# Kernel tuning notes

Measured on AMD Instinct MI355X. Metric: run time of the kernel, lower is better.

Reference implementation:

```python
import jax, jax.numpy as jnp
import numpy as np

B, A, G, C, P, PH, PW = 8, 19248, 32, 81, 32, 138, 138
K_POS = 128            # fixed upper bound on positives used for the mask loss
INPUT_SIZE = 550.0
POS_THR, NEG_THR = 0.5, 0.4
ALPHA, GAMMA = 0.25, 2.0
NEG_POS_RATIO = 3
CLS_W, BOX_W, MASK_W = 1.0, 1.5, 6.125
VAR_XY, VAR_WH = 0.1, 0.2
EPS = 1e-6


def setup_inputs() -> dict:
    key = jax.random.key(0)
    ks = jax.random.split(key, 10)
    class_preds = jax.random.normal(ks[0], (B, A, C), jnp.float32)
    box_preds = jax.random.normal(ks[1], (B, A, 4), jnp.float32) * 0.1
    mask_coeffs = jax.random.normal(ks[2], (B, A, P), jnp.float32)
    prototypes = jax.random.normal(ks[3], (B, P, PH, PW), jnp.float32)
    # anchors in normalized [cx, cy, w, h]
    cxy = jax.random.uniform(ks[4], (A, 2), jnp.float32)
    wh = jax.random.uniform(ks[5], (A, 2), jnp.float32) * 0.25 + 0.02
    anchors = jnp.concatenate([cxy, wh], axis=-1)
    # GT boxes in absolute pixels [x1, y1, x2, y2] within 550x550
    xy1 = jax.random.uniform(ks[6], (B, G, 2), jnp.float32) * 380.0
    bwh = jax.random.uniform(ks[7], (B, G, 2), jnp.float32) * 150.0 + 15.0
    gt_boxes = jnp.concatenate([xy1, xy1 + bwh], axis=-1)
    gt_labels = jax.random.randint(ks[8], (B, G), 1, C)  # foreground classes
    gt_masks = (jax.random.uniform(ks[9], (B, G, PH, PW)) > 0.5).astype(jnp.float32)
    return {
        "class_preds": class_preds, "box_preds": box_preds,
        "mask_coeffs": mask_coeffs, "prototypes": prototypes,
        "anchors": anchors, "gt_boxes": gt_boxes,
        "gt_labels": gt_labels, "gt_masks": gt_masks,
    }


def _iou(a, b):
    # a: (A,4) xyxy, b: (G,4) xyxy -> (A,G)
    max_xy = jnp.minimum(a[:, None, 2:], b[None, :, 2:])
    min_xy = jnp.maximum(a[:, None, :2], b[None, :, :2])
    inter = jnp.clip(max_xy - min_xy, 0.0).prod(-1)
    area_a = (a[:, 2] - a[:, 0]) * (a[:, 3] - a[:, 1])
    area_b = (b[:, 2] - b[:, 0]) * (b[:, 3] - b[:, 1])
    union = area_a[:, None] + area_b[None, :] - inter
    return inter / jnp.clip(union, EPS)


def _smooth_l1(x):
    d = jnp.abs(x)
    return jnp.where(d < 1.0, 0.5 * d * d, d - 0.5)


def _image_loss(cls_p, box_p, coeffs, protos, gtb, gtl, gtm, anchors, anchors_xyxy):
    gtb = gtb / INPUT_SIZE                           # normalize to [0,1]
    iou = _iou(anchors_xyxy, gtb)                    # (A, G)
    best_gt_iou = iou.max(axis=1)                    # (A,)
    best_gt_idx = iou.argmax(axis=1)                 # (A,)
    best_anchor_idx = iou.argmax(axis=0)             # (G,) bipartite guarantee

    pos = best_gt_iou >= POS_THR
    pos = pos.at[best_anchor_idx].set(True)
    best_gt_idx = best_gt_idx.at[best_anchor_idx].set(jnp.arange(G))
    neg = (best_gt_iou < NEG_THR) & ~pos
    num_pos = pos.sum()
    # deterministic hard-negative cap at neg:pos = 3:1 (orig. uses randperm)
    neg = neg & (jnp.cumsum(neg) <= num_pos * NEG_POS_RATIO)

    matched_labels = jnp.where(pos, gtl[best_gt_idx], 0)   # 0 = background
    mb = gtb[best_gt_idx]                                  # (A,4) matched xyxy
    posf = pos.astype(jnp.float32)

    # ---- focal classification loss over pos|neg anchors ----
    probs = jax.nn.softmax(cls_p, axis=-1)
    p_t = jnp.take_along_axis(probs, matched_labels[:, None], axis=1)[:, 0]
    p_t = jnp.clip(p_t, EPS, 1.0 - EPS)
    alpha_t = jnp.where(matched_labels > 0, ALPHA, 1.0 - ALPHA)
    focal = alpha_t * (1.0 - p_t) ** GAMMA * (-jnp.log(p_t))
    cls_loss = (focal * (pos | neg).astype(jnp.float32)).sum()

    acx, acy, aw, ah = anchors[:, 0], anchors[:, 1], anchors[:, 2], anchors[:, 3]
    gcx = 0.5 * (mb[:, 0] + mb[:, 2]); gcy = 0.5 * (mb[:, 1] + mb[:, 3])
    gw = jnp.clip(mb[:, 2] - mb[:, 0], EPS); gh = jnp.clip(mb[:, 3] - mb[:, 1], EPS)
    t = jnp.stack([
        (gcx - acx) / (aw * VAR_XY),
        (gcy - acy) / (ah * VAR_XY),
        jnp.log(gw / aw) / VAR_WH,
        jnp.log(gh / ah) / VAR_WH,
    ], axis=-1)                                            # (A,4)
    box_loss = (_smooth_l1(box_p - t).sum(-1) * posf).sum()

    # ---- BCE mask loss on (up to K_POS) positive anchors ----
    score = jnp.where(pos, best_gt_iou + 1.0, 0.0)
    _, idx = jax.lax.top_k(score, K_POS)                   # (K,)
    w = posf[idx]                                          # 0-weight padding
    logits = jnp.einsum('kp,phw->khw', coeffs[idx], protos)  # (K,PH,PW)
    tgt = gtm[best_gt_idx[idx]]                            # (K,PH,PW)
    bce = jnp.maximum(logits, 0.0) - logits * tgt + jnp.log1p(jnp.exp(-jnp.abs(logits)))
    mask_loss = (bce.mean(axis=(1, 2)) * w).sum()

    return cls_loss, box_loss, mask_loss, num_pos


def reference(class_preds, box_preds, mask_coeffs, prototypes, anchors, gt_boxes, gt_labels, gt_masks):
    a_xyxy = jnp.concatenate(
        [anchors[:, :2] - anchors[:, 2:] * 0.5, anchors[:, :2] + anchors[:, 2:] * 0.5], axis=-1)
    cls_l, box_l, mask_l, npos = jax.vmap(
        _image_loss, in_axes=(0, 0, 0, 0, 0, 0, 0, None, None)
    )(class_preds, box_preds, mask_coeffs, prototypes, gt_boxes, gt_labels, gt_masks, anchors, a_xyxy)
    denom = jnp.maximum(npos.sum(), 1).astype(jnp.float32)
    total = (CLS_W * cls_l.sum() + BOX_W * box_l.sum() + MASK_W * mask_l.sum()) / denom
    return total
```

## Files before the change

### kernel.cpp

```cpp
#include <hip/hip_runtime.h>
#include <math.h>

#define BB 8
#define AA 19248
#define GG 32
#define CC 81
#define PP 32
#define PHW 19044
#define KPOS 128
#define NEGRATIO 3
#define SELCAP 7680
#define NWCH 304
#define NB1 76
#define NB0 75
#define NPT 1191
#define NB7 298
#define NB45 24

typedef _Float16 half8 __attribute__((ext_vector_type(8)));
typedef float floatx4 __attribute__((ext_vector_type(4)));

__device__ __forceinline__ float iou_one(float ax1, float ay1, float ax2, float ay2,
                                         float areaA,
                                         float gx1, float gy1, float gx2, float gy2) {
#pragma clang fp contract(off)
    float ix1 = fmaxf(ax1, gx1), iy1 = fmaxf(ay1, gy1);
    float ix2 = fminf(ax2, gx2), iy2 = fminf(ay2, gy2);
    float iw = fmaxf(ix2 - ix1, 0.0f), ih = fmaxf(iy2 - iy1, 0.0f);
    float inter = iw * ih;
    float areaB = (gx2 - gx1) * (gy2 - gy1);
    float u = areaA + areaB - inter;
    u = fmaxf(u, 1e-6f);
    return inter / u;
}

__global__ __launch_bounds__(256) void k01(
    const float* __restrict__ anchors, const float* __restrict__ gt_boxes,
    const float* __restrict__ protos, const float* __restrict__ gtm,
    float* __restrict__ best_iou, int* __restrict__ best_g,
    unsigned long long* __restrict__ gkey_part, float* __restrict__ acc,
    _Float16* __restrict__ protoT, unsigned* __restrict__ pmask) {
#pragma clang fp contract(off)
    int b = blockIdx.y;
    __shared__ float sg[GG][4];
    __shared__ unsigned long long s_gk[GG];

    if (blockIdx.x >= NB1) {
        int px = (blockIdx.x - NB1) * 256 + threadIdx.x;
        if (px >= PHW) return;
        const float* pb = protos + (size_t)b * PP * PHW + px;
        _Float16 v[PP];
        #pragma unroll
        for (int k = 0; k < PP; ++k)
            v[k] = (_Float16)pb[(size_t)k * PHW];
        half8* dst = (half8*)&protoT[((size_t)b * PHW + px) * PP];
        #pragma unroll
        for (int q = 0; q < 4; ++q)
            dst[q] = *(half8*)&v[q * 8];
        const float* gb = gtm + (size_t)b * GG * PHW + px;
        unsigned m = 0u;
        #pragma unroll
        for (int g = 0; g < GG; ++g)
            m |= (gb[(size_t)g * PHW] > 0.5f) ? (1u << g) : 0u;
        pmask[(size_t)b * PHW + px] = m;
        return;
    }

    int a = blockIdx.x * 256 + threadIdx.x;
    int lane = threadIdx.x & 63;
    if (blockIdx.x == 0 && b == 0 && threadIdx.x < 4)
        ((int*)acc)[threadIdx.x] = 0;
    for (int t = threadIdx.x; t < GG * 4; t += 256)
        sg[t >> 2][t & 3] = gt_boxes[b * GG * 4 + t] / 550.0f;
    if (threadIdx.x < GG) s_gk[threadIdx.x] = 0ULL;
    __syncthreads();
    bool valid = a < AA;
    int ac = valid ? a : AA - 1;
    float4 an = ((const float4*)anchors)[ac];
    float ax1 = an.x - an.z * 0.5f, ay1 = an.y - an.w * 0.5f;
    float ax2 = an.x + an.z * 0.5f, ay2 = an.y + an.w * 0.5f;
    float areaA = (ax2 - ax1) * (ay2 - ay1);
    unsigned long long bk = 0ULL;
    for (int gg = 0; gg < GG; ++gg) {
        int g = (gg + lane) & (GG - 1);
        float v = iou_one(ax1, ay1, ax2, ay2, areaA, sg[g][0], sg[g][1], sg[g][2], sg[g][3]);
        unsigned vb = __float_as_uint(v);
        unsigned long long k2 = ((unsigned long long)vb << 6) | (unsigned)(GG - 1 - g);
        if (k2 > bk) bk = k2;
        if (valid) {
            unsigned long long kg =
                ((unsigned long long)vb << 32) | (unsigned)(AA - 1 - a);
            atomicMax(&s_gk[g], kg);
        }
    }
    if (valid) {
        best_iou[b * AA + a] = __uint_as_float((unsigned)(bk >> 6));
        best_g[b * AA + a] = (GG - 1) - (int)(bk & 63ULL);
    }
    __syncthreads();
    if (threadIdx.x < GG)
        gkey_part[((size_t)b * NB1 + blockIdx.x) * GG + threadIdx.x] = s_gk[threadIdx.x];
}

__global__ __launch_bounds__(1024) void k36(
    const float* __restrict__ best_iou, const int* __restrict__ best_g_in,
    const unsigned long long* __restrict__ gkey_part, const int* __restrict__ gtl,
    int* __restrict__ gidx_out, int* __restrict__ selmask,
    unsigned long long* __restrict__ pos_key,
    int* __restrict__ pos_cnt, int* __restrict__ g_npos,
    int* __restrict__ act_list, int* __restrict__ act_cnt,
    const float* __restrict__ coeffs,
    int* __restrict__ sel_g, _Float16* __restrict__ sel_coef,
    int* __restrict__ sel_cnt) {
#pragma clang fp contract(off)
    int b = blockIdx.x;
    int tid = threadIdx.x;
    int lane = tid & 63, wid = tid >> 6;
    __shared__ short s_ov[AA];
    __shared__ unsigned long long s_gmax[GG];
    __shared__ int sba[GG];
    __shared__ int s_gtl[GG];
    __shared__ unsigned long long s_pmask[NWCH];
    __shared__ unsigned long long s_nmask[NWCH];
    __shared__ int s_woff[NWCH];
    __shared__ int s_wred[5];
    __shared__ int s_cnt, s_act;
    __shared__ unsigned long long s_keys[SELCAP];
    __shared__ int s_hist[256];
    __shared__ int s_sfx[256];
    __shared__ int s_wsum[4];
    __shared__ unsigned long long s_prefix;
    __shared__ int s_kk;
    __shared__ int s_nsel;
    __shared__ int s_sel_a[KPOS];
    __shared__ int s_sorted_a[KPOS];
    __shared__ int s_sorted_g[KPOS];
    __shared__ int s_gcnt[GG];

    for (int i = tid; i < AA; i += 1024) s_ov[i] = -1;
    if (tid < GG) { s_gmax[tid] = 0ULL; s_gtl[tid] = gtl[b * GG + tid]; }
    if (tid == 0) { s_cnt = 0; s_act = 0; s_prefix = 0ULL; s_kk = KPOS; s_nsel = 0; }
    __syncthreads();
    for (int c = tid >> 5; c < NB1; c += 32)
        atomicMax(&s_gmax[tid & 31],
                  gkey_part[((size_t)b * NB1 + c) * GG + (tid & 31)]);
    __syncthreads();
    if (tid < GG) sba[tid] = AA - 1 - (int)(unsigned)(s_gmax[tid] & 0xffffffffULL);
    __syncthreads();
    if (tid == 0) {
        for (int g = 0; g < GG; ++g) s_ov[sba[g]] = (short)g;
    }
    __syncthreads();

    for (int base = 0; base < AA; base += 1024) {
        int a = base + tid;
        bool p = false, npre = false;
        if (a < AA) {
            float biou = best_iou[b * AA + a];
            int ov = s_ov[a];
            int gi = (ov >= 0) ? ov : best_g_in[b * AA + a];
            p = (biou >= 0.5f) || (ov >= 0);
            npre = (biou < 0.4f) && !p;
            gidx_out[b * AA + a] = gi;
            selmask[b * AA + a] = p ? 2 : (npre ? 1 : 0);
            if (p) {
                int slot = atomicAdd(&s_cnt, 1);
                unsigned vb = __float_as_uint(biou + 1.0f);
                unsigned long long key =
                    ((unsigned long long)(vb - 0x3F800000u) << 32) |
                    (unsigned)(AA - 1 - a);
                pos_key[(size_t)b * AA + slot] = key;
                if (slot < SELCAP) s_keys[slot] = key;
            }
        }
        unsigned long long pm = __ballot(p);
        unsigned long long nm = __ballot(npre);
        if (lane == 0) {
            int w = (base >> 6) + wid;
            s_pmask[w] = pm;
            s_nmask[w] = nm;
        }
    }
    __syncthreads();
    int npos = s_cnt;
    if (tid == 0) { pos_cnt[b] = npos; atomicAdd(g_npos, npos); }
    int cap = npos * NEGRATIO;

    int c = (tid < NWCH) ? __popcll(s_nmask[tid]) : 0;
    int inc = c;
    if (wid < 5) {
        #pragma unroll
        for (int d = 1; d < 64; d <<= 1) {
            int t = __shfl_up(inc, d);
            if (lane >= d) inc += t;
        }
        if (lane == 63) s_wred[wid] = inc;
    }
    __syncthreads();
    if (tid == 0) {
        int run = 0;
        #pragma unroll
        for (int i = 0; i < 5; ++i) { int t = s_wred[i]; s_wred[i] = run; run += t; }
    }
    __syncthreads();
    if (tid < NWCH) s_woff[tid] = inc - c + s_wred[wid];
    __syncthreads();

    for (int base = 0; base < AA; base += 1024) {
        int a = base + tid;
        int w = (base >> 6) + wid;
        unsigned long long nm = s_nmask[w], pm = s_pmask[w];
        bool npre = (nm >> lane) & 1ULL;
        bool pos  = (pm >> lane) & 1ULL;
        int rank = __popcll(nm & ((1ULL << lane) - 1ULL));
        bool kept = npre && (s_woff[w] + rank + 1 <= cap);
        if (a < AA) {
            if (npre && !kept) selmask[b * AA + a] = 0;
            if (pos || kept) {
                int slot = atomicAdd(&s_act, 1);
                int gi = gidx_out[b * AA + a];
                int lbl = pos ? s_gtl[gi] : 0;
                unsigned e = (unsigned)a | ((unsigned)gi << 15) |
                             ((unsigned)lbl << 20) | (pos ? 0x80000000u : 0u);
                act_list[b * AA + slot] = (int)e;
            }
        }
    }
    __syncthreads();
    if (tid == 0) act_cnt[b] = s_act;

    int n = npos;
    int K = (n < KPOS) ? n : KPOS;
    const unsigned long long* keys =
        (n <= SELCAP) ? s_keys : (pos_key + (size_t)b * AA);
    __syncthreads();

    if (n > KPOS) {
        for (int d = 6; d >= 0; --d) {
            unsigned long long pref = s_prefix;
            int kk = s_kk;
            if (tid < 256) s_hist[tid] = 0;
            __syncthreads();
            unsigned long long mhi = ~((1ULL << (8 * (d + 1))) - 1ULL);
            for (int i = tid; i < n; i += 1024) {
                unsigned long long k = keys[i];
                if ((k & mhi) == pref)
                    atomicAdd(&s_hist[(int)((k >> (8 * d)) & 255)], 1);
            }
            __syncthreads();
            int x = 0;
            if (tid < 256) {
                x = s_hist[255 - tid];
                #pragma unroll
                for (int o = 1; o < 64; o <<= 1) {
                    int t = __shfl_up(x, o);
                    if (lane >= o) x += t;
                }
                if (lane == 63) s_wsum[tid >> 6] = x;
            }
            __syncthreads();
            if (tid == 0) {
                int run = 0;
                #pragma unroll
                for (int i = 0; i < 4; ++i) { int t = s_wsum[i]; s_wsum[i] = run; run += t; }
            }
            __syncthreads();
            if (tid < 256) s_sfx[255 - tid] = x + s_wsum[tid >> 6];
            __syncthreads();
            if (tid < 256) {
                int v = tid;
                int ge = s_sfx[v];
                int gt = (v == 255) ? 0 : s_sfx[v + 1];
                if (ge >= kk && gt < kk) {
                    s_prefix = pref | ((unsigned long long)v << (8 * d));
                    s_kk = kk - gt;
                }
            }
            __syncthreads();
        }
    }

    unsigned long long T = (n > KPOS) ? s_prefix : 0ULL;
    for (int i = tid; i < n; i += 1024) {
        unsigned long long k = keys[i];
        if (k >= T) {
            int slot = atomicAdd(&s_nsel, 1);
            if (slot < KPOS)
                s_sel_a[slot] = AA - 1 - (int)(unsigned)(k & 0xffffffffu);
        }
    }
    __syncthreads();

    if (tid < GG) s_gcnt[tid] = 0;
    __syncthreads();
    int mya = -1, myg = -1;
    if (tid < K) {
        mya = s_sel_a[tid];
        myg = gidx_out[b * AA + mya];
        atomicAdd(&s_gcnt[myg], 1);
    }
    __syncthreads();
    if (tid == 0) {
        int run = 0;
        for (int g = 0; g < GG; ++g) { int cg = s_gcnt[g]; s_gcnt[g] = run; run += cg; }
    }
    __syncthreads();
    if (tid < K) {
        int pos = atomicAdd(&s_gcnt[myg], 1);
        s_sorted_a[pos] = mya;
        s_sorted_g[pos] = myg;
    }
    __syncthreads();

    if (tid == 0) sel_cnt[b] = K;
    int glast = (K > 0) ? s_sorted_g[K - 1] : 0;
    for (int t = tid; t < KPOS * PP; t += 1024) {
        int k = t >> 5, p = t & 31;
        _Float16 v = (_Float16)0.0f;
        if (k < K) {
            int a = s_sorted_a[k];
            v = (_Float16)coeffs[((size_t)(b * AA + a)) * PP + p];
        }
        sel_coef[(size_t)(b * KPOS + k) * PP + p] = v;
    }
    for (int t = tid; t < KPOS; t += 1024)
        sel_g[b * KPOS + t] = (t < K) ? s_sorted_g[t] : glast;
}

__global__ __launch_bounds__(256) void k457(
    const float* __restrict__ cls_p, const int* __restrict__ act_list,
    const int* __restrict__ act_cnt, const float* __restrict__ box_p,
    const float* __restrict__ anchors, const float* __restrict__ gt_boxes,
    float* __restrict__ part_cls, float* __restrict__ part_box,
    const _Float16* __restrict__ protoT, const unsigned* __restrict__ pmask,
    const _Float16* __restrict__ sel_coef, const int* __restrict__ sel_g,
    const int* __restrict__ sel_cnt, float* __restrict__ part_mask) {
    int b = blockIdx.y;
    int tid = threadIdx.x;

    if (blockIdx.x < NB45) {
        int n = act_cnt[b];
        float fsum = 0.0f, bsum = 0.0f;
        for (int i = blockIdx.x * 256 + tid; i < n; i += NB45 * 256) {
            unsigned e = (unsigned)act_list[b * AA + i];
            int a = e & 0x7fff;
            int g = (e >> 15) & 31;
            int lbl = (e >> 20) & 127;
            bool pos = (e >> 31) != 0u;
            const float* x = cls_p + (size_t)(b * AA + a) * CC;
            float v80 = x[80];
            float m0 = v80, m1 = -3.0e38f, m2 = -3.0e38f, m3 = -3.0e38f;
            #pragma unroll
            for (int q = 0; q < 20; ++q) {
                m0 = fmaxf(m0, x[4 * q + 0]); m1 = fmaxf(m1, x[4 * q + 1]);
                m2 = fmaxf(m2, x[4 * q + 2]); m3 = fmaxf(m3, x[4 * q + 3]);
            }
            float m = fmaxf(fmaxf(m0, m1), fmaxf(m2, m3));
            float s0 = __expf(v80 - m), s1 = 0.f, s2 = 0.f, s3 = 0.f;
            #pragma unroll
            for (int q = 0; q < 20; ++q) {
                s0 += __expf(x[4 * q + 0] - m); s1 += __expf(x[4 * q + 1] - m);
                s2 += __expf(x[4 * q + 2] - m); s3 += __expf(x[4 * q + 3] - m);
            }
            float s = (s0 + s1) + (s2 + s3);
            float pt = __expf(x[lbl] - m) / s;
            pt = fminf(fmaxf(pt, 1e-6f), 1.0f - 1e-6f);
            float at = (lbl > 0) ? 0.25f : 0.75f;
            float om = 1.0f - pt;
            fsum += at * om * om * (-__logf(pt));
            if (pos) {
#pragma clang fp contract(off)
                float4 mb = ((const float4*)gt_boxes)[b * GG + g];
                float4 an = ((const float4*)anchors)[a];
                const float4 bp = ((const float4*)box_p)[(size_t)b * AA + a];
                float q0 = mb.x / 550.0f, q1 = mb.y / 550.0f;
                float q2 = mb.z / 550.0f, q3 = mb.w / 550.0f;
                float gcx = 0.5f * (q0 + q2), gcy = 0.5f * (q1 + q3);
                float gw = fmaxf(q2 - q0, 1e-6f), gh = fmaxf(q3 - q1, 1e-6f);
                float t0 = (gcx - an.x) / (an.z * 0.1f);
                float t1 = (gcy - an.y) / (an.w * 0.1f);
                float t2 = logf(gw / an.z) / 0.2f;
                float t3 = logf(gh / an.w) / 0.2f;
                float d;
                d = fabsf(bp.x - t0); bsum += (d < 1.0f) ? 0.5f * d * d : d - 0.5f;
                d = fabsf(bp.y - t1); bsum += (d < 1.0f) ? 0.5f * d * d : d - 0.5f;
                d = fabsf(bp.z - t2); bsum += (d < 1.0f) ? 0.5f * d * d : d - 0.5f;
                d = fabsf(bp.w - t3); bsum += (d < 1.0f) ? 0.5f * d * d : d - 0.5f;
            }
        }
        for (int off = 32; off; off >>= 1) {
            fsum += __shfl_xor(fsum, off);
            bsum += __shfl_xor(bsum, off);
        }
        __shared__ float s4f[4], s4b[4];
        if ((tid & 63) == 0) { s4f[tid >> 6] = fsum; s4b[tid >> 6] = bsum; }
        __syncthreads();
        if (tid == 0) {
            part_cls[b * NB45 + blockIdx.x] = s4f[0] + s4f[1] + s4f[2] + s4f[3];
            part_box[b * NB45 + blockIdx.x] = s4b[0] + s4b[1] + s4b[2] + s4b[3];
        }
        return;
    }

    int nk = sel_cnt[b];
    int wave = tid >> 6, lane = tid & 63;
    int lg = lane >> 4;
    int ln = lane & 15;
    int pt = (blockIdx.x - NB45) * 4 + wave;
    int px = pt * 16 + ln;
    bool pxv = (pt < NPT) && (px < PHW);
    int pc = pxv ? px : PHW - 1;

    half8 bfrag = *(const half8*)&protoT[((size_t)b * PHW + pc) * PP + lg * 8];
    unsigned gmask = pmask[(size_t)b * PHW + pc];

    const _Float16* ca = sel_coef + (size_t)b * KPOS * PP;
    const int* gb = sel_g + b * KPOS;

    half8 af[8];
    int4 gv[8];
    #pragma unroll
    for (int kt = 0; kt < 8; ++kt) {
        af[kt] = *(const half8*)&ca[(size_t)(kt * 16 + ln) * PP + lg * 8];
        gv[kt] = *(const int4*)&gb[kt * 16 + lg * 4];
    }

    float acc = 0.0f;
    #pragma unroll
    for (int kt = 0; kt < 8; ++kt) {
        floatx4 c = {0.f, 0.f, 0.f, 0.f};
        c = __builtin_amdgcn_mfma_f32_16x16x32_f16(af[kt], bfrag, c, 0, 0, 0);
        #pragma unroll
        for (int r = 0; r < 4; ++r) {
            int k = kt * 16 + lg * 4 + r;
            float l = c[r];
            int g0 = (r == 0) ? gv[kt].x : (r == 1) ? gv[kt].y
                   : (r == 2) ? gv[kt].z : gv[kt].w;
            float t = (float)((gmask >> g0) & 1u);
            float bce = fmaxf(l, 0.f) - l * t + __logf(1.f + __expf(-fabsf(l)));
            if (pxv && k < nk) acc += bce;
        }
    }

    for (int off = 32; off; off >>= 1) acc += __shfl_xor(acc, off);
    __shared__ float s_red[4];
    if (lane == 0) s_red[wave] = acc;
    __syncthreads();
    if (tid == 0)
        part_mask[(size_t)b * NB7 + (blockIdx.x - NB45)] =
            s_red[0] + s_red[1] + s_red[2] + s_red[3];
}

__global__ __launch_bounds__(1024) void k8_final(
    const float* __restrict__ part_cls, const float* __restrict__ part_box,
    const float* __restrict__ part_mask, const int* __restrict__ npos,
    float* __restrict__ out) {
    int tid = threadIdx.x;
    float c = 0.f, bx = 0.f, mk = 0.f;
    for (int i = tid; i < NB45 * BB; i += 1024) {
        c += part_cls[i];
        bx += part_box[i];
    }
    for (int i = tid; i < NB7 * BB; i += 1024)
        mk += part_mask[i];
    for (int off = 32; off; off >>= 1) {
        c += __shfl_xor(c, off);
        bx += __shfl_xor(bx, off);
        mk += __shfl_xor(mk, off);
    }
    __shared__ float sc[16], sb[16], sm[16];
    if ((tid & 63) == 0) {
        sc[tid >> 6] = c; sb[tid >> 6] = bx; sm[tid >> 6] = mk;
    }
    __syncthreads();
    if (tid == 0) {
        float tc = 0.f, tb = 0.f, tm = 0.f;
        #pragma unroll
        for (int i = 0; i < 16; ++i) { tc += sc[i]; tb += sb[i]; tm += sm[i]; }
        float denom = fmaxf((float)(*npos), 1.0f);
        out[0] = (1.0f * tc + 1.5f * tb + 6.125f * (tm / (float)PHW)) / denom;
    }
}

extern "C" void kernel_launch(void* const* d_in, const int* in_sizes, int n_in,
                              void* d_out, int out_size, void* d_ws, size_t ws_size,
                              hipStream_t stream) {
    (void)in_sizes; (void)n_in; (void)out_size; (void)ws_size;
    const float* class_preds = (const float*)d_in[0];
    const float* box_preds   = (const float*)d_in[1];
    const float* mask_coeffs = (const float*)d_in[2];
    const float* prototypes  = (const float*)d_in[3];
    const float* anchors     = (const float*)d_in[4];
    const float* gt_boxes    = (const float*)d_in[5];
    const int*   gt_labels   = (const int*)d_in[6];
    const float* gt_masks    = (const float*)d_in[7];
    float* out = (float*)d_out;

    size_t off = 0;
    char* w = (char*)d_ws;
    auto take = [&](size_t bytes) -> char* {
        char* p = w + off;
        off += (bytes + 255) & ~(size_t)255;
        return p;
    };
    float* acc      = (float*)take(32);
    float* best_iou = (float*)take((size_t)BB * AA * 4);
    int*   best_g   = (int*)  take((size_t)BB * AA * 4);
    int*   gidx     = (int*)  take((size_t)BB * AA * 4);
    int*   selmask  = (int*)  take((size_t)BB * AA * 4);
    unsigned long long* gkey_part =
        (unsigned long long*)take((size_t)BB * NB1 * GG * 8);
    int*   pos_cnt  = (int*)  take((size_t)BB * 4);
    unsigned long long* pos_key = (unsigned long long*)take((size_t)BB * AA * 8);
    int*   sel_g    = (int*)  take((size_t)BB * KPOS * 4);
    int*   sel_cnt  = (int*)  take((size_t)BB * 4);
    _Float16* sel_coef = (_Float16*)take((size_t)BB * KPOS * PP * 2);
    int*   act_list = (int*)  take((size_t)BB * AA * 4);
    int*   act_cnt  = (int*)  take((size_t)BB * 4);
    _Float16* protoT = (_Float16*)take((size_t)BB * PHW * PP * 2);
    unsigned* pmaskb = (unsigned*)take((size_t)BB * PHW * 4);
    float* part_cls  = (float*)take((size_t)BB * NB45 * 4);
    float* part_box  = (float*)take((size_t)BB * NB45 * 4);
    float* part_mask = (float*)take((size_t)BB * NB7 * 4);

    k01<<<dim3(NB1 + NB0, BB), 256, 0, stream>>>(
        anchors, gt_boxes, prototypes, gt_masks,
        best_iou, best_g, gkey_part, acc, protoT, pmaskb);
    k36<<<BB, 1024, 0, stream>>>(
        best_iou, best_g, gkey_part, gt_labels, gidx, selmask, pos_key, pos_cnt,
        (int*)(acc + 3), act_list, act_cnt,
        mask_coeffs, sel_g, sel_coef, sel_cnt);
    k457<<<dim3(NB45 + NB7, BB), 256, 0, stream>>>(
        class_preds, act_list, act_cnt, box_preds, anchors, gt_boxes,
        part_cls, part_box,
        protoT, pmaskb, sel_coef, sel_g, sel_cnt, part_mask);
    k8_final<<<1, 1024, 0, stream>>>(
        part_cls, part_box, part_mask, (int*)(acc + 3), out);
}
```

Before: 71.96 us.

## Pack best IoU/gt into one key, keep gt index in LDS, fold final reduction

k01 now writes a single 64-bit packed key per anchor instead of separate best_iou and best_g arrays. k36 keeps the matched gt index in shared memory and drops the global gidx and selmask arrays and the shared key cache. The final reduction kernel is removed; the last k457 block, detected through an atomic done counter, does the final sum. This cuts global traffic and one kernel launch, but top-k selection now always reads keys from global memory.

```diff
diff --git a/kernel.cpp b/kernel.cpp
--- a/kernel.cpp
+++ b/kernel.cpp
@@ -9,13 +9,13 @@
 #define PHW 19044
 #define KPOS 128
 #define NEGRATIO 3
-#define SELCAP 7680
 #define NWCH 304
 #define NB1 76
 #define NB0 75
 #define NPT 1191
 #define NB7 298
 #define NB45 24
+#define NTOT ((NB45 + NB7) * BB)
 
 typedef _Float16 half8 __attribute__((ext_vector_type(8)));
 typedef float floatx4 __attribute__((ext_vector_type(4)));
@@ -37,7 +37,7 @@
 __global__ __launch_bounds__(256) void k01(
     const float* __restrict__ anchors, const float* __restrict__ gt_boxes,
     const float* __restrict__ protos, const float* __restrict__ gtm,
-    float* __restrict__ best_iou, int* __restrict__ best_g,
+    unsigned long long* __restrict__ best_key,
     unsigned long long* __restrict__ gkey_part, float* __restrict__ acc,
     _Float16* __restrict__ protoT, unsigned* __restrict__ pmask) {
 #pragma clang fp contract(off)
@@ -93,30 +93,27 @@
             atomicMax(&s_gk[g], kg);
         }
     }
-    if (valid) {
-        best_iou[b * AA + a] = __uint_as_float((unsigned)(bk >> 6));
-        best_g[b * AA + a] = (GG - 1) - (int)(bk & 63ULL);
-    }
+    if (valid) best_key[(size_t)b * AA + a] = bk;
     __syncthreads();
     if (threadIdx.x < GG)
         gkey_part[((size_t)b * NB1 + blockIdx.x) * GG + threadIdx.x] = s_gk[threadIdx.x];
 }
 
 __global__ __launch_bounds__(1024) void k36(
-    const float* __restrict__ best_iou, const int* __restrict__ best_g_in,
+    const unsigned long long* __restrict__ best_key,
     const unsigned long long* __restrict__ gkey_part, const int* __restrict__ gtl,
-    int* __restrict__ gidx_out, int* __restrict__ selmask,
     unsigned long long* __restrict__ pos_key,
     int* __restrict__ pos_cnt, int* __restrict__ g_npos,
     int* __restrict__ act_list, int* __restrict__ act_cnt,
     const float* __restrict__ coeffs,
     int* __restrict__ sel_g, _Float16* __restrict__ sel_coef,
-    int* __restrict__ sel_cnt) {
+    int* __restrict__ sel_cnt, int* __restrict__ done_ctr) {
 #pragma clang fp contract(off)
     int b = blockIdx.x;
     int tid = threadIdx.x;
     int lane = tid & 63, wid = tid >> 6;
     __shared__ short s_ov[AA];
+    __shared__ short s_gi[AA];
     __shared__ unsigned long long s_gmax[GG];
     __shared__ int sba[GG];
     __shared__ int s_gtl[GG];
@@ -125,7 +122,6 @@
     __shared__ int s_woff[NWCH];
     __shared__ int s_wred[5];
     __shared__ int s_cnt, s_act;
-    __shared__ unsigned long long s_keys[SELCAP];
     __shared__ int s_hist[256];
     __shared__ int s_sfx[256];
     __shared__ int s_wsum[4];
@@ -139,7 +135,10 @@
 
     for (int i = tid; i < AA; i += 1024) s_ov[i] = -1;
     if (tid < GG) { s_gmax[tid] = 0ULL; s_gtl[tid] = gtl[b * GG + tid]; }
-    if (tid == 0) { s_cnt = 0; s_act = 0; s_prefix = 0ULL; s_kk = KPOS; s_nsel = 0; }
+    if (tid == 0) {
+        s_cnt = 0; s_act = 0; s_prefix = 0ULL; s_kk = KPOS; s_nsel = 0;
+        if (b == 0) *done_ctr = 0;
+    }
     __syncthreads();
     for (int c = tid >> 5; c < NB1; c += 32)
         atomicMax(&s_gmax[tid & 31],
@@ -156,13 +155,14 @@
         int a = base + tid;
         bool p = false, npre = false;
         if (a < AA) {
-            float biou = best_iou[b * AA + a];
+            unsigned long long bk = best_key[(size_t)b * AA + a];
+            float biou = __uint_as_float((unsigned)(bk >> 6));
+            int bg = (GG - 1) - (int)(bk & 63ULL);
             int ov = s_ov[a];
-            int gi = (ov >= 0) ? ov : best_g_in[b * AA + a];
+            int gi = (ov >= 0) ? ov : bg;
             p = (biou >= 0.5f) || (ov >= 0);
             npre = (biou < 0.4f) && !p;
-            gidx_out[b * AA + a] = gi;
-            selmask[b * AA + a] = p ? 2 : (npre ? 1 : 0);
+            s_gi[a] = (short)gi;
             if (p) {
                 int slot = atomicAdd(&s_cnt, 1);
                 unsigned vb = __float_as_uint(biou + 1.0f);
@@ -170,7 +170,6 @@
                     ((unsigned long long)(vb - 0x3F800000u) << 32) |
                     (unsigned)(AA - 1 - a);
                 pos_key[(size_t)b * AA + slot] = key;
-                if (slot < SELCAP) s_keys[slot] = key;
             }
         }
         unsigned long long pm = __ballot(p);
@@ -214,16 +213,13 @@
         bool pos  = (pm >> lane) & 1ULL;
         int rank = __popcll(nm & ((1ULL << lane) - 1ULL));
         bool kept = npre && (s_woff[w] + rank + 1 <= cap);
-        if (a < AA) {
-            if (npre && !kept) selmask[b * AA + a] = 0;
-            if (pos || kept) {
-                int slot = atomicAdd(&s_act, 1);
-                int gi = gidx_out[b * AA + a];
-                int lbl = pos ? s_gtl[gi] : 0;
-                unsigned e = (unsigned)a | ((unsigned)gi << 15) |
-                             ((unsigned)lbl << 20) | (pos ? 0x80000000u : 0u);
-                act_list[b * AA + slot] = (int)e;
-            }
+        if (a < AA && (pos || kept)) {
+            int slot = atomicAdd(&s_act, 1);
+            int gi = s_gi[a];
+            int lbl = pos ? s_gtl[gi] : 0;
+            unsigned e = (unsigned)a | ((unsigned)gi << 15) |
+                         ((unsigned)lbl << 20) | (pos ? 0x80000000u : 0u);
+            act_list[b * AA + slot] = (int)e;
         }
     }
     __syncthreads();
@@ -231,8 +227,7 @@
 
     int n = npos;
     int K = (n < KPOS) ? n : KPOS;
-    const unsigned long long* keys =
-        (n <= SELCAP) ? s_keys : (pos_key + (size_t)b * AA);
+    const unsigned long long* keys = pos_key + (size_t)b * AA;
     __syncthreads();
 
     if (n > KPOS) {
@@ -296,7 +291,7 @@
     int mya = -1, myg = -1;
     if (tid < K) {
         mya = s_sel_a[tid];
-        myg = gidx_out[b * AA + mya];
+        myg = s_gi[mya];
         atomicAdd(&s_gcnt[myg], 1);
     }
     __syncthreads();
@@ -334,9 +329,13 @@
     float* __restrict__ part_cls, float* __restrict__ part_box,
     const _Float16* __restrict__ protoT, const unsigned* __restrict__ pmask,
     const _Float16* __restrict__ sel_coef, const int* __restrict__ sel_g,
-    const int* __restrict__ sel_cnt, float* __restrict__ part_mask) {
+    const int* __restrict__ sel_cnt, float* __restrict__ part_mask,
+    const int* __restrict__ npos, int* __restrict__ done_ctr,
+    float* __restrict__ out) {
     int b = blockIdx.y;
     int tid = threadIdx.x;
+    __shared__ float s4f[4], s4b[4];
+    __shared__ int s_last;
 
     if (blockIdx.x < NB45) {
         int n = act_cnt[b];
@@ -392,91 +391,89 @@
             fsum += __shfl_xor(fsum, off);
             bsum += __shfl_xor(bsum, off);
         }
-        __shared__ float s4f[4], s4b[4];
         if ((tid & 63) == 0) { s4f[tid >> 6] = fsum; s4b[tid >> 6] = bsum; }
         __syncthreads();
         if (tid == 0) {
             part_cls[b * NB45 + blockIdx.x] = s4f[0] + s4f[1] + s4f[2] + s4f[3];
             part_box[b * NB45 + blockIdx.x] = s4b[0] + s4b[1] + s4b[2] + s4b[3];
         }
-        return;
-    }
-
-    int nk = sel_cnt[b];
-    int wave = tid >> 6, lane = tid & 63;
-    int lg = lane >> 4;
-    int ln = lane & 15;
-    int pt = (blockIdx.x - NB45) * 4 + wave;
-    int px = pt * 16 + ln;
-    bool pxv = (pt < NPT) && (px < PHW);
-    int pc = pxv ? px : PHW - 1;
-
-    half8 bfrag = *(const half8*)&protoT[((size_t)b * PHW + pc) * PP + lg * 8];
-    unsigned gmask = pmask[(size_t)b * PHW + pc];
-
-    const _Float16* ca = sel_coef + (size_t)b * KPOS * PP;
-    const int* gb = sel_g + b * KPOS;
-
-    half8 af[8];
-    int4 gv[8];
-    #pragma unroll
-    for (int kt = 0; kt < 8; ++kt) {
-        af[kt] = *(const half8*)&ca[(size_t)(kt * 16 + ln) * PP + lg * 8];
-        gv[kt] = *(const int4*)&gb[kt * 16 + lg * 4];
-    }
-
-    float acc = 0.0f;
-    #pragma unroll
-    for (int kt = 0; kt < 8; ++kt) {
-        floatx4 c = {0.f, 0.f, 0.f, 0.f};
-        c = __builtin_amdgcn_mfma_f32_16x16x32_f16(af[kt], bfrag, c, 0, 0, 0);
-        #pragma unroll
-        for (int r = 0; r < 4; ++r) {
-            int k = kt * 16 + lg * 4 + r;
-            float l = c[r];
-            int g0 = (r == 0) ? gv[kt].x : (r == 1) ? gv[kt].y
-                   : (r == 2) ? gv[kt].z : gv[kt].w;
-            float t = (float)((gmask >> g0) & 1u);
-            float bce = fmaxf(l, 0.f) - l * t + __logf(1.f + __expf(-fabsf(l)));
-            if (pxv && k < nk) acc += bce;
-        }
-    }
-
-    for (int off = 32; off; off >>= 1) acc += __shfl_xor(acc, off);
-    __shared__ float s_red[4];
-    if (lane == 0) s_red[wave] = acc;
-    __syncthreads();
-    if (tid == 0)
-        part_mask[(size_t)b * NB7 + (blockIdx.x - NB45)] =
-            s_red[0] + s_red[1] + s_red[2] + s_red[3];
-}
-
-__global__ __launch_bounds__(1024) void k8_final(
-    const float* __restrict__ part_cls, const float* __restrict__ part_box,
-    const float* __restrict__ part_mask, const int* __restrict__ npos,
-    float* __restrict__ out) {
-    int tid = threadIdx.x;
+    } else {
+        int nk = sel_cnt[b];
+        int wave = tid >> 6, lane = tid & 63;
+        int lg = lane >> 4;
+        int ln = lane & 15;
+        int pt = (blockIdx.x - NB45) * 4 + wave;
+        int px = pt * 16 + ln;
+        bool pxv = (pt < NPT) && (px < PHW);
+        int pc = pxv ? px : PHW - 1;
+
+        half8 bfrag = *(const half8*)&protoT[((size_t)b * PHW + pc) * PP + lg * 8];
+        unsigned gmask = pmask[(size_t)b * PHW + pc];
+
+        const _Float16* ca = sel_coef + (size_t)b * KPOS * PP;
+        const int* gb = sel_g + b * KPOS;
+
+        half8 af[8];
+        int4 gv[8];
+        #pragma unroll
+        for (int kt = 0; kt < 8; ++kt) {
+            af[kt] = *(const half8*)&ca[(size_t)(kt * 16 + ln) * PP + lg * 8];
+            gv[kt] = *(const int4*)&gb[kt * 16 + lg * 4];
+        }
+
+        float acc = 0.0f;
+        #pragma unroll
+        for (int kt = 0; kt < 8; ++kt) {
+            floatx4 c = {0.f, 0.f, 0.f, 0.f};
+            c = __builtin_amdgcn_mfma_f32_16x16x32_f16(af[kt], bfrag, c, 0, 0, 0);
+            #pragma unroll
+            for (int r = 0; r < 4; ++r) {
+                int k = kt * 16 + lg * 4 + r;
+                float l = c[r];
+                int g0 = (r == 0) ? gv[kt].x : (r == 1) ? gv[kt].y
+                       : (r == 2) ? gv[kt].z : gv[kt].w;
+                float t = (float)((gmask >> g0) & 1u);
+                float bce = fmaxf(l, 0.f) - l * t + __logf(1.f + __expf(-fabsf(l)));
+                if (pxv && k < nk) acc += bce;
+            }
+        }
+
+        for (int off = 32; off; off >>= 1) acc += __shfl_xor(acc, off);
+        if (lane == 0) s4f[wave] = acc;
+        __syncthreads();
+        if (tid == 0)
+            part_mask[(size_t)b * NB7 + (blockIdx.x - NB45)] =
+                s4f[0] + s4f[1] + s4f[2] + s4f[3];
+    }
+
+    if (tid == 0) {
+        __threadfence();
+        int t = atomicAdd(done_ctr, 1);
+        s_last = (t == NTOT - 1) ? 1 : 0;
+    }
+    __syncthreads();
+    if (!s_last) return;
+    __threadfence();
+
     float c = 0.f, bx = 0.f, mk = 0.f;
-    for (int i = tid; i < NB45 * BB; i += 1024) {
+    for (int i = tid; i < NB45 * BB; i += 256) {
         c += part_cls[i];
         bx += part_box[i];
     }
-    for (int i = tid; i < NB7 * BB; i += 1024)
+    for (int i = tid; i < NB7 * BB; i += 256)
         mk += part_mask[i];
     for (int off = 32; off; off >>= 1) {
         c += __shfl_xor(c, off);
         bx += __shfl_xor(bx, off);
         mk += __shfl_xor(mk, off);
     }
-    __shared__ float sc[16], sb[16], sm[16];
-    if ((tid & 63) == 0) {
-        sc[tid >> 6] = c; sb[tid >> 6] = bx; sm[tid >> 6] = mk;
-    }
+    __shared__ float rc[4], rb[4], rm[4];
+    if ((tid & 63) == 0) { rc[tid >> 6] = c; rb[tid >> 6] = bx; rm[tid >> 6] = mk; }
     __syncthreads();
     if (tid == 0) {
-        float tc = 0.f, tb = 0.f, tm = 0.f;
-        #pragma unroll
-        for (int i = 0; i < 16; ++i) { tc += sc[i]; tb += sb[i]; tm += sm[i]; }
+        float tc = rc[0] + rc[1] + rc[2] + rc[3];
+        float tb = rb[0] + rb[1] + rb[2] + rb[3];
+        float tm = rm[0] + rm[1] + rm[2] + rm[3];
         float denom = fmaxf((float)(*npos), 1.0f);
         out[0] = (1.0f * tc + 1.5f * tb + 6.125f * (tm / (float)PHW)) / denom;
     }
@@ -504,10 +501,9 @@
         return p;
     };
     float* acc      = (float*)take(32);
-    float* best_iou = (float*)take((size_t)BB * AA * 4);
-    int*   best_g   = (int*)  take((size_t)BB * AA * 4);
-    int*   gidx     = (int*)  take((size_t)BB * AA * 4);
-    int*   selmask  = (int*)  take((size_t)BB * AA * 4);
+    int*   done_ctr = (int*)  take(256);
+    unsigned long long* best_key =
+        (unsigned long long*)take((size_t)BB * AA * 8);
     unsigned long long* gkey_part =
         (unsigned long long*)take((size_t)BB * NB1 * GG * 8);
     int*   pos_cnt  = (int*)  take((size_t)BB * 4);
@@ -525,15 +521,13 @@
 
     k01<<<dim3(NB1 + NB0, BB), 256, 0, stream>>>(
         anchors, gt_boxes, prototypes, gt_masks,
-        best_iou, best_g, gkey_part, acc, protoT, pmaskb);
+        best_key, gkey_part, acc, protoT, pmaskb);
     k36<<<BB, 1024, 0, stream>>>(
-        best_iou, best_g, gkey_part, gt_labels, gidx, selmask, pos_key, pos_cnt,
-        (int*)(acc + 3), act_list, act_cnt,
-        mask_coeffs, sel_g, sel_coef, sel_cnt);
+        best_key, gkey_part, gt_labels, pos_key, pos_cnt, (int*)(acc + 3),
+        act_list, act_cnt, mask_coeffs, sel_g, sel_coef, sel_cnt, done_ctr);
     k457<<<dim3(NB45 + NB7, BB), 256, 0, stream>>>(
         class_preds, act_list, act_cnt, box_preds, anchors, gt_boxes,
         part_cls, part_box,
-        protoT, pmaskb, sel_coef, sel_g, sel_cnt, part_mask);
-    k8_final<<<1, 1024, 0, stream>>>(
-        part_cls, part_box, part_mask, (int*)(acc + 3), out);
+        protoT, pmaskb, sel_coef, sel_g, sel_cnt, part_mask,
+        (int*)(acc + 3), done_ctr, out);
 }
```

Result: slower. 124.7 us (+73.3%).
